# Kernel optimization log

Hardware: AMD Instinct MI355X
Metric: run time of the kernel (lower is better)

## Reference

```python
import jax, jax.numpy as jnp
import numpy as np

START_INDEX = 1


def _lstm_cell(x, h, c, W_ih, W_hh, b_ih, b_hh):
    # PyTorch LSTM cell: gate order i, f, g, o
    gates = x @ W_ih.T + b_ih + h @ W_hh.T + b_hh  # [B, 4H]
    i, f, g, o = jnp.split(gates, 4, axis=-1)
    c_new = jax.nn.sigmoid(f) * c + jax.nn.sigmoid(i) * jnp.tanh(g)
    h_new = jax.nn.sigmoid(o) * jnp.tanh(c_new)
    return h_new, c_new


def setup_inputs() -> dict:
    key = jax.random.key(0)
    ks = jax.random.split(key, 13)
    B, C, E, H, V = 32, 512, 512, 512, 32000
    s = 0.05  # keep gates in non-saturated range

    def w(k, shape):
        return jax.random.normal(k, shape, dtype=jnp.float32) * s

    return {
        "context": jax.random.normal(ks[0], (B, C), dtype=jnp.float32),
        "emb": w(ks[1], (V, E)),
        "W_ih_l0": w(ks[2], (4 * H, E + C)),
        "W_hh_l0": w(ks[3], (4 * H, H)),
        "b_ih_l0": w(ks[4], (4 * H,)),
        "b_hh_l0": w(ks[5], (4 * H,)),
        "W_ih_l1": w(ks[6], (4 * H, H)),
        "W_hh_l1": w(ks[7], (4 * H, H)),
        "b_ih_l1": w(ks[8], (4 * H,)),
        "b_hh_l1": w(ks[9], (4 * H,)),
        "W_out": w(ks[10], (V, H)),
        "b_out": w(ks[11], (V,)),
        "max_len": 64,
    }


def reference(context, emb, W_ih_l0, W_hh_l0, b_ih_l0, b_hh_l0,
              W_ih_l1, W_hh_l1, b_ih_l1, b_hh_l1, W_out, b_out, max_len):
    B = context.shape[0]
    H = W_hh_l0.shape[1]
    tok0 = jnp.full((B,), START_INDEX, dtype=jnp.int32)
    z = jnp.zeros((B, H), dtype=context.dtype)

    def step(carry, _):
        tok, h0, c0, h1, c1 = carry
        ex = emb[tok]                                   # [B, E] embedding lookup
        inp = jnp.concatenate([ex, context], axis=-1)   # [B, E+C]
        h0, c0 = _lstm_cell(inp, h0, c0, W_ih_l0, W_hh_l0, b_ih_l0, b_hh_l0)
        h1, c1 = _lstm_cell(h0, h1, c1, W_ih_l1, W_hh_l1, b_ih_l1, b_hh_l1)
        logits = h1 @ W_out.T + b_out                   # [B, V]
        logp = jax.nn.log_softmax(logits, axis=-1)
        tok_next = jnp.argmax(logp, axis=-1).astype(jnp.int32)  # greedy feedback (detached)
        return (tok_next, h0, c0, h1, c1), logp

    _, out = jax.lax.scan(step, (tok0, z, z, z, z), None, length=max_len)
    return jnp.transpose(out, (1, 0, 2))                # [B, max_len, V]
```

## Files before the change

kernel.cpp:

```cpp
#include <hip/hip_runtime.h>
#include <math.h>

#define BB 32
#define HH 512
#define VV 32000
#define TT 64
#define NTILE 1000

#define OFF_H0T   0
#define OFF_H1T   32768
#define OFF_C0    65536
#define OFF_C1    81920
#define OFF_PC0   98304
#define OFF_AMAX  163840
#define OFF_PAIRS 163904

typedef float f32x4_ __attribute__((ext_vector_type(4)));

__device__ __forceinline__ float sigmoidf_(float x) { return 1.0f / (1.0f + expf(-x)); }

__device__ __forceinline__ float dot4(const float4 wv, const float4 xv) {
    return wv.x * xv.x + wv.y * xv.y + wv.z * xv.z + wv.w * xv.w;
}
__device__ __forceinline__ void bcast_fma(float* A, const float4 wv,
                                          const float4 x0, const float4 x1,
                                          const float4 x2, const float4 x3) {
    A[0] += wv.x * x0.x + wv.y * x1.x + wv.z * x2.x + wv.w * x3.x;
    A[1] += wv.x * x0.y + wv.y * x1.y + wv.z * x2.y + wv.w * x3.y;
    A[2] += wv.x * x0.z + wv.y * x1.z + wv.z * x2.z + wv.w * x3.z;
    A[3] += wv.x * x0.w + wv.y * x1.w + wv.z * x2.w + wv.w * x3.w;
}

__global__ void k_init(float* __restrict__ ws) {
    int idx = blockIdx.x * 256 + threadIdx.x;
    ws[OFF_H0T + idx] = 0.0f;
    ws[OFF_H1T + idx] = 0.0f;
    ws[OFF_C0 + idx]  = 0.0f;
    ws[OFF_C1 + idx]  = 0.0f;
    if (idx < BB) ((unsigned long long*)(ws + OFF_AMAX))[idx] = 0xFFFFFFFEull;
}

__global__ __launch_bounds__(256, 4) void k_pc0(
    const float* __restrict__ Wih0, const float* __restrict__ ctx,
    const float* __restrict__ bih0, const float* __restrict__ bhh0,
    float* __restrict__ pc0)
{
    __shared__ float red[16][16][32];
    const int tid = threadIdx.x;
    const int ks = tid >> 4, bg = (tid >> 2) & 3, rg = tid & 3;
    const int hu = blockIdx.x * 4 + rg;
    const int k0 = ks * 32, b0 = bg * 8;

    float acc[4][8];
#pragma unroll
    for (int g = 0; g < 4; ++g)
#pragma unroll
        for (int j = 0; j < 8; ++j) acc[g][j] = 0.0f;

    const float* wp[4];
#pragma unroll
    for (int g = 0; g < 4; ++g) wp[g] = Wih0 + (size_t)(g * 512 + hu) * 1024 + 512 + k0;

#pragma unroll 2
    for (int kk4 = 0; kk4 < 8; ++kk4) {
        const int kk = kk4 * 4;
        float4 w4[4];
#pragma unroll
        for (int g = 0; g < 4; ++g) w4[g] = *(const float4*)(wp[g] + kk);
#pragma unroll
        for (int j = 0; j < 8; ++j) {
            const float4 xe = *(const float4*)(ctx + (size_t)(b0 + j) * 512 + k0 + kk);
#pragma unroll
            for (int g = 0; g < 4; ++g) acc[g][j] += dot4(w4[g], xe);
        }
    }

#pragma unroll
    for (int g = 0; g < 4; ++g) {
        *(float4*)&red[ks][g * 4 + rg][b0]     = make_float4(acc[g][0], acc[g][1], acc[g][2], acc[g][3]);
        *(float4*)&red[ks][g * 4 + rg][b0 + 4] = make_float4(acc[g][4], acc[g][5], acc[g][6], acc[g][7]);
    }
    __syncthreads();
    if (tid < 128) {
        const int huL = (tid >> 5) & 3, b = tid & 31;
#pragma unroll
        for (int g = 0; g < 4; ++g) {
            float s = 0.0f;
#pragma unroll
            for (int k = 0; k < 16; ++k) s += red[k][g * 4 + huL][b];
            const int row = g * 512 + blockIdx.x * 4 + huL;
            pc0[(size_t)row * 32 + b] = s + bih0[row] + bhh0[row];
        }
    }
}

template <int MODE>
__global__ __launch_bounds__(256, 4) void k_lstm(
    const float* __restrict__ Wa, const float* __restrict__ Wb,
    const float* __restrict__ xA, const float* __restrict__ xB,
    const float* __restrict__ emb,
    const unsigned long long* __restrict__ amax_in,
    const float* __restrict__ pc0,
    const float* __restrict__ bih, const float* __restrict__ bhh,
    float* __restrict__ hT_out, float* __restrict__ c_st,
    unsigned long long* __restrict__ amax_reset)
{
    constexpr int SA = (MODE == 0) ? 1024 : 512;
    __shared__ float red[16][8][32];

    const int tid = threadIdx.x;
    const int ks = tid >> 4, bg = (tid >> 1) & 7, rg = tid & 1;
    const int hu = blockIdx.x * 2 + rg;
    const int b0 = bg * 4;
    const bool partA = (ks < 8);
    const int k0 = (partA ? ks : ks - 8) * 64;

    float acc[4][4];
#pragma unroll
    for (int g = 0; g < 4; ++g)
#pragma unroll
        for (int j = 0; j < 4; ++j) acc[g][j] = 0.0f;

    const float* wp[4];
#pragma unroll
    for (int g = 0; g < 4; ++g)
        wp[g] = partA ? (Wa + (size_t)(g * 512 + hu) * SA + k0)
                      : (Wb + (size_t)(g * 512 + hu) * 512 + k0);

    const float* ep[4];
    if (MODE == 0 && partA) {
#pragma unroll
        for (int j = 0; j < 4; ++j) {
            const int tok = (int)(0xFFFFFFFFu - (unsigned)(amax_in[b0 + j] & 0xFFFFFFFFull));
            ep[j] = emb + (size_t)tok * 512 + k0;
        }
    }
    const float* xb = (partA ? xA : xB) + (size_t)k0 * 32 + b0;

#pragma unroll 2
    for (int kk4 = 0; kk4 < 16; ++kk4) {
        const int kk = kk4 * 4;
        float4 w4[4];
#pragma unroll
        for (int g = 0; g < 4; ++g) w4[g] = *(const float4*)(wp[g] + kk);
        if (MODE == 0 && partA) {
#pragma unroll
            for (int j = 0; j < 4; ++j) {
                const float4 xe = *(const float4*)(ep[j] + kk);
#pragma unroll
                for (int g = 0; g < 4; ++g) acc[g][j] += dot4(w4[g], xe);
            }
        } else {
            const float4 x0 = *(const float4*)(xb + (size_t)(kk + 0) * 32);
            const float4 x1 = *(const float4*)(xb + (size_t)(kk + 1) * 32);
            const float4 x2 = *(const float4*)(xb + (size_t)(kk + 2) * 32);
            const float4 x3 = *(const float4*)(xb + (size_t)(kk + 3) * 32);
#pragma unroll
            for (int g = 0; g < 4; ++g) bcast_fma(acc[g], w4[g], x0, x1, x2, x3);
        }
    }

#pragma unroll
    for (int g = 0; g < 4; ++g)
        *(float4*)&red[ks][g * 2 + rg][b0] = make_float4(acc[g][0], acc[g][1], acc[g][2], acc[g][3]);
    __syncthreads();

    if (tid < 64) {
        const int huL = tid >> 5, b = tid & 31;
        const int hu2 = blockIdx.x * 2 + huL;
        float gate[4];
#pragma unroll
        for (int g = 0; g < 4; ++g) {
            float s = 0.0f;
#pragma unroll
            for (int k = 0; k < 16; ++k) s += red[k][g * 2 + huL][b];
            const int row = g * 512 + hu2;
            if (MODE == 0) s += pc0[(size_t)row * 32 + b];
            else           s += bih[row] + bhh[row];
            gate[g] = s;
        }
        const float gi = sigmoidf_(gate[0]);
        const float gf = sigmoidf_(gate[1]);
        const float gg = tanhf(gate[2]);
        const float go = sigmoidf_(gate[3]);
        const int ci = hu2 * 32 + b;
        const float cn = gf * c_st[ci] + gi * gg;
        c_st[ci] = cn;
        hT_out[ci] = go * tanhf(cn);
    }
    if (MODE == 1) {
        if (tid >= 64 && tid < 96) amax_reset[tid - 64] = 0ull;
    }
}

__global__ __launch_bounds__(256, 4) void k_logits(
    const float* __restrict__ h1T, const float* __restrict__ Wout,
    const float* __restrict__ bout, float* __restrict__ out,
    unsigned long long* __restrict__ amax, float* __restrict__ pairs, int t)
{
    __shared__ float red[8][32][36];
    __shared__ unsigned long long lmax[8][32];
    __shared__ float pm[8][32], ps[8][32];

    const int tid = threadIdx.x;
    const int rg = tid & 7, bg = (tid >> 3) & 3, ks = tid >> 5;
    const int row0 = blockIdx.x * 32 + rg * 4;
    const int b0 = bg * 8, k0 = ks * 64;

    float acc[4][8];
#pragma unroll
    for (int i = 0; i < 4; ++i)
#pragma unroll
        for (int j = 0; j < 8; ++j) acc[i][j] = 0.0f;

    const float* wp[4];
#pragma unroll
    for (int i = 0; i < 4; ++i) wp[i] = Wout + (size_t)(row0 + i) * 512 + k0;
    const float* xb = h1T + (size_t)k0 * 32 + b0;

#pragma unroll 2
    for (int kk4 = 0; kk4 < 16; ++kk4) {
        const int kk = kk4 * 4;
        const float4 x00 = *(const float4*)(xb + (size_t)(kk + 0) * 32);
        const float4 x01 = *(const float4*)(xb + (size_t)(kk + 0) * 32 + 4);
        const float4 x10 = *(const float4*)(xb + (size_t)(kk + 1) * 32);
        const float4 x11 = *(const float4*)(xb + (size_t)(kk + 1) * 32 + 4);
        const float4 x20 = *(const float4*)(xb + (size_t)(kk + 2) * 32);
        const float4 x21 = *(const float4*)(xb + (size_t)(kk + 2) * 32 + 4);
        const float4 x30 = *(const float4*)(xb + (size_t)(kk + 3) * 32);
        const float4 x31 = *(const float4*)(xb + (size_t)(kk + 3) * 32 + 4);
#pragma unroll
        for (int i = 0; i < 4; ++i) {
            const float4 w = *(const float4*)(wp[i] + kk);
            bcast_fma(&acc[i][0], w, x00, x10, x20, x30);
            bcast_fma(&acc[i][4], w, x01, x11, x21, x31);
        }
    }

#pragma unroll
    for (int i = 0; i < 4; ++i) {
        *(float4*)&red[ks][rg * 4 + i][b0]     = make_float4(acc[i][0], acc[i][1], acc[i][2], acc[i][3]);
        *(float4*)&red[ks][rg * 4 + i][b0 + 4] = make_float4(acc[i][4], acc[i][5], acc[i][6], acc[i][7]);
    }
    __syncthreads();

    {
        const int r2 = tid & 31, bq = tid >> 5;
        const int row = blockIdx.x * 32 + r2;
        const float bias = bout[row];
#pragma unroll
        for (int j = 0; j < 4; ++j) {
            const int b = bq * 4 + j;
            float v = bias;
#pragma unroll
            for (int k = 0; k < 8; ++k) v += red[k][r2][b];
            out[((size_t)b * TT + t) * VV + row] = v;
        }
    }
    {
        const int b = tid & 31, rq = tid >> 5;
        unsigned long long best = 0ull;
        float vv[4];
#pragma unroll
        for (int i = 0; i < 4; ++i) {
            const int rr = rq * 4 + i;
            const int row = blockIdx.x * 32 + rr;
            float v = bout[row];
#pragma unroll
            for (int k = 0; k < 8; ++k) v += red[k][rr][b];
            vv[i] = v;
            unsigned u = __float_as_uint(v);
            u = (u & 0x80000000u) ? ~u : (u | 0x80000000u);
            const unsigned long long key =
                ((unsigned long long)u << 32) | (unsigned long long)(0xFFFFFFFFu - (unsigned)row);
            best = best > key ? best : key;
        }
        lmax[rq][b] = best;
        const float lm = fmaxf(fmaxf(vv[0], vv[1]), fmaxf(vv[2], vv[3]));
        ps[rq][b] = __expf(vv[0] - lm) + __expf(vv[1] - lm)
                  + __expf(vv[2] - lm) + __expf(vv[3] - lm);
        pm[rq][b] = lm;
    }
    __syncthreads();
    if (tid < 32) {
        unsigned long long bb = lmax[0][tid];
#pragma unroll
        for (int q = 1; q < 8; ++q) bb = bb > lmax[q][tid] ? bb : lmax[q][tid];
        if (bb > amax[tid]) atomicMax(&amax[tid], bb);
        if (pairs) {
            float M = pm[0][tid], S = ps[0][tid];
#pragma unroll
            for (int q = 1; q < 8; ++q) {
                const float nm = fmaxf(M, pm[q][tid]);
                S = S * __expf(M - nm) + ps[q][tid] * __expf(pm[q][tid] - nm);
                M = nm;
            }
            float* pr = pairs + ((size_t)t * NTILE + blockIdx.x) * 64;
            pr[tid] = M;
            pr[32 + tid] = S;
        }
    }
}

__global__ __launch_bounds__(256) void k_lsm(float* __restrict__ out,
                                             const float* __restrict__ pairs) {
    float* p = out + (size_t)blockIdx.x * VV;
    const int tid = threadIdx.x;
    __shared__ float sm[4], ss[4];

    float m = -1e30f, s = 0.0f;
    if (pairs) {
        const int b = blockIdx.x >> 6, t = blockIdx.x & 63;
        const float* pr = pairs + (size_t)t * NTILE * 64 + b;
        for (int tile = tid; tile < NTILE; tile += 256) {
            const float tm = pr[(size_t)tile * 64];
            const float ts = pr[(size_t)tile * 64 + 32];
            const float nm = fmaxf(m, tm);
            s = s * __expf(m - nm) + ts * __expf(tm - nm);
            m = nm;
        }
    } else {
        for (int i = tid * 4; i < VV; i += 1024) {
            const float4 v = *(const float4*)(p + i);
            const float cm = fmaxf(fmaxf(v.x, v.y), fmaxf(v.z, v.w));
            const float nm = fmaxf(m, cm);
            s = s * __expf(m - nm) + __expf(v.x - nm) + __expf(v.y - nm)
                                   + __expf(v.z - nm) + __expf(v.w - nm);
            m = nm;
        }
    }
#pragma unroll
    for (int off = 32; off > 0; off >>= 1) {
        const float om = __shfl_down(m, off, 64);
        const float os = __shfl_down(s, off, 64);
        const float nm = fmaxf(m, om);
        s = s * __expf(m - nm) + os * __expf(om - nm);
        m = nm;
    }
    if ((tid & 63) == 0) { sm[tid >> 6] = m; ss[tid >> 6] = s; }
    __syncthreads();
    float M = sm[0], S = ss[0];
#pragma unroll
    for (int w = 1; w < 4; ++w) {
        const float nm = fmaxf(M, sm[w]);
        S = S * __expf(M - nm) + ss[w] * __expf(sm[w] - nm);
        M = nm;
    }
    const float lz = M + __logf(S);
    for (int i = tid * 4; i < VV; i += 1024) {
        f32x4_ v = *(const f32x4_*)(p + i);
        v = v - lz;
        __builtin_nontemporal_store(v, (f32x4_*)(p + i));
    }
}

extern "C" void kernel_launch(void* const* d_in, const int* in_sizes, int n_in,
                              void* d_out, int out_size, void* d_ws, size_t ws_size,
                              hipStream_t stream) {
    const float* ctx  = (const float*)d_in[0];
    const float* emb  = (const float*)d_in[1];
    const float* Wih0 = (const float*)d_in[2];
    const float* Whh0 = (const float*)d_in[3];
    const float* bih0 = (const float*)d_in[4];
    const float* bhh0 = (const float*)d_in[5];
    const float* Wih1 = (const float*)d_in[6];
    const float* Whh1 = (const float*)d_in[7];
    const float* bih1 = (const float*)d_in[8];
    const float* bhh1 = (const float*)d_in[9];
    const float* Wout = (const float*)d_in[10];
    const float* bout = (const float*)d_in[11];

    float* out = (float*)d_out;
    float* ws  = (float*)d_ws;
    float* h0T[2] = { ws + OFF_H0T, ws + OFF_H0T + 16384 };
    float* h1T[2] = { ws + OFF_H1T, ws + OFF_H1T + 16384 };
    float* c0  = ws + OFF_C0;
    float* c1  = ws + OFF_C1;
    float* pc0 = ws + OFF_PC0;
    unsigned long long* amax = (unsigned long long*)(ws + OFF_AMAX);

    const size_t need_bytes = (size_t)(OFF_PAIRS + TT * NTILE * 64) * sizeof(float);
    float* pairs = (ws_size >= need_bytes) ? (ws + OFF_PAIRS) : nullptr;

    k_init<<<64, 256, 0, stream>>>(ws);
    k_pc0<<<128, 256, 0, stream>>>(Wih0, ctx, bih0, bhh0, pc0);

    for (int t = 0; t < TT; ++t) {
        const int pp = t & 1, nn = pp ^ 1;
        k_lstm<0><<<256, 256, 0, stream>>>(
            Wih0, Whh0, nullptr, h0T[pp], emb, amax, pc0, nullptr, nullptr,
            h0T[nn], c0, nullptr);
        k_lstm<1><<<256, 256, 0, stream>>>(
            Wih1, Whh1, h0T[nn], h1T[pp], emb, nullptr, nullptr, bih1, bhh1,
            h1T[nn], c1, amax);
        k_logits<<<1000, 256, 0, stream>>>(h1T[nn], Wout, bout, out, amax, pairs, t);
    }
    k_lsm<<<BB * TT, 256, 0, stream>>>(out, pairs);
}
```

Before: 5.452 ms.

## Fuse per-step decode kernels into one persistent kernel with grid barriers

Replaces the 192 per-timestep launches (two LSTM layers plus logits, 64 steps) with a single persistent 256-block kernel. The three phases are separated by a custom flag-based global barrier, and the argmax buffer is double-buffered so no reset kernel is needed. The LSTM and logits tiling is remapped to 512-thread blocks with wavefront shuffle reductions in place of shared-memory reductions. The logits phase uses 250 blocks of 128 rows and fuses the partial softmax statistics. The aim is to remove launch overhead and inter-kernel gaps. The costs are spin-wait barrier latency, reliance on all 256 blocks being co-resident, and fewer blocks for the large Wout GEMV.

```diff
diff --git a/kernel.cpp b/kernel.cpp
--- a/kernel.cpp
+++ b/kernel.cpp
@@ -5,15 +5,20 @@
 #define HH 512
 #define VV 32000
 #define TT 64
-#define NTILE 1000
+#define GRID 256
+#define NLOG 250
+#define RPB 128
+
+typedef unsigned long long ull;
 
 #define OFF_H0T   0
 #define OFF_H1T   32768
 #define OFF_C0    65536
 #define OFF_C1    81920
 #define OFF_PC0   98304
-#define OFF_AMAX  163840
-#define OFF_PAIRS 163904
+#define OFF_AMAX2 163840
+#define OFF_BAR   163968
+#define OFF_PAIRS 164480
 
 typedef float f32x4_ __attribute__((ext_vector_type(4)));
 
@@ -37,7 +42,10 @@
     ws[OFF_H1T + idx] = 0.0f;
     ws[OFF_C0 + idx]  = 0.0f;
     ws[OFF_C1 + idx]  = 0.0f;
-    if (idx < BB) ((unsigned long long*)(ws + OFF_AMAX))[idx] = 0xFFFFFFFEull;
+    if (idx < 64) {
+        ((ull*)(ws + OFF_AMAX2))[idx] = (idx < 32) ? 0xFFFFFFFEull : 0ull;
+    }
+    if (idx < 512) ((unsigned*)(ws + OFF_BAR))[idx] = 0u;
 }
 
 __global__ __launch_bounds__(256, 4) void k_pc0(
@@ -94,26 +102,49 @@
     }
 }
 
+__device__ __forceinline__ void gbar(unsigned* flags, unsigned* done, unsigned target) {
+    __syncthreads();
+    if (threadIdx.x == 0) {
+        __threadfence();
+        atomicExch(&flags[blockIdx.x], target);
+    }
+    if (blockIdx.x == 0 && threadIdx.x < 64) {
+#pragma unroll
+        for (int i = 0; i < GRID / 64; ++i) {
+            unsigned* f = &flags[i * 64 + threadIdx.x];
+            while (atomicAdd(f, 0u) < target) __builtin_amdgcn_s_sleep(1);
+        }
+        if (threadIdx.x < 4) atomicExch(&done[threadIdx.x * 32], target);
+    }
+    if (threadIdx.x == 0 && blockIdx.x != 0) {
+        unsigned* d = &done[(blockIdx.x & 3) * 32];
+        while (atomicAdd(d, 0u) < target) __builtin_amdgcn_s_sleep(1);
+    }
+    if (threadIdx.x == 0) __threadfence();
+    __syncthreads();
+}
+
 template <int MODE>
-__global__ __launch_bounds__(256, 4) void k_lstm(
+__device__ __forceinline__ void lstm_phase(
+    const int blk, const int tid,
     const float* __restrict__ Wa, const float* __restrict__ Wb,
     const float* __restrict__ xA, const float* __restrict__ xB,
     const float* __restrict__ emb,
-    const unsigned long long* __restrict__ amax_in,
+    const ull* __restrict__ amax_rd,
     const float* __restrict__ pc0,
     const float* __restrict__ bih, const float* __restrict__ bhh,
     float* __restrict__ hT_out, float* __restrict__ c_st,
-    unsigned long long* __restrict__ amax_reset)
+    ull* __restrict__ amax_zero,
+    float (*__restrict__ part)[4][32])
 {
     constexpr int SA = (MODE == 0) ? 1024 : 512;
-    __shared__ float red[16][8][32];
-
-    const int tid = threadIdx.x;
-    const int ks = tid >> 4, bg = (tid >> 1) & 7, rg = tid & 1;
-    const int hu = blockIdx.x * 2 + rg;
-    const int b0 = bg * 4;
-    const bool partA = (ks < 8);
-    const int k0 = (partA ? ks : ks - 8) * 64;
+    const int w = tid >> 6, lane = tid & 63, ks = lane >> 3, bq = lane & 7;
+    const int hu = blk * 2 + (w & 1);
+    const int c  = w >> 1;
+    const int k0 = c * 256 + ks * 32;
+    const bool partA = (k0 < 512);
+    const int ka = partA ? k0 : k0 - 512;
+    const int b0 = bq * 4;
 
     float acc[4][4];
 #pragma unroll
@@ -124,21 +155,21 @@
     const float* wp[4];
 #pragma unroll
     for (int g = 0; g < 4; ++g)
-        wp[g] = partA ? (Wa + (size_t)(g * 512 + hu) * SA + k0)
-                      : (Wb + (size_t)(g * 512 + hu) * 512 + k0);
+        wp[g] = partA ? (Wa + (size_t)(g * 512 + hu) * SA + ka)
+                      : (Wb + (size_t)(g * 512 + hu) * 512 + ka);
 
     const float* ep[4];
     if (MODE == 0 && partA) {
 #pragma unroll
         for (int j = 0; j < 4; ++j) {
-            const int tok = (int)(0xFFFFFFFFu - (unsigned)(amax_in[b0 + j] & 0xFFFFFFFFull));
-            ep[j] = emb + (size_t)tok * 512 + k0;
-        }
-    }
-    const float* xb = (partA ? xA : xB) + (size_t)k0 * 32 + b0;
-
-#pragma unroll 2
-    for (int kk4 = 0; kk4 < 16; ++kk4) {
+            const int tok = (int)(0xFFFFFFFFu - (unsigned)(amax_rd[b0 + j] & 0xFFFFFFFFull));
+            ep[j] = emb + (size_t)tok * 512 + ka;
+        }
+    }
+    const float* xp = (partA ? xA : xB) + (size_t)ka * 32 + b0;
+
+#pragma unroll
+    for (int kk4 = 0; kk4 < 8; ++kk4) {
         const int kk = kk4 * 4;
         float4 w4[4];
 #pragma unroll
@@ -151,154 +182,187 @@
                 for (int g = 0; g < 4; ++g) acc[g][j] += dot4(w4[g], xe);
             }
         } else {
+            const float4 x0 = *(const float4*)(xp + (size_t)(kk + 0) * 32);
+            const float4 x1 = *(const float4*)(xp + (size_t)(kk + 1) * 32);
+            const float4 x2 = *(const float4*)(xp + (size_t)(kk + 2) * 32);
+            const float4 x3 = *(const float4*)(xp + (size_t)(kk + 3) * 32);
+#pragma unroll
+            for (int g = 0; g < 4; ++g) bcast_fma(acc[g], w4[g], x0, x1, x2, x3);
+        }
+    }
+
+#pragma unroll
+    for (int off = 8; off <= 32; off <<= 1)
+#pragma unroll
+        for (int g = 0; g < 4; ++g)
+#pragma unroll
+            for (int j = 0; j < 4; ++j)
+                acc[g][j] += __shfl_xor(acc[g][j], off, 64);
+
+    if (ks < 4)
+        *(float4*)&part[w][ks][b0] = make_float4(acc[ks][0], acc[ks][1], acc[ks][2], acc[ks][3]);
+
+    if (MODE == 0 && blk == GRID - 1 && tid >= 64 && tid < 96)
+        amax_zero[tid - 64] = 0ull;
+
+    __syncthreads();
+
+    if (tid < 64) {
+        const int hl = tid >> 5, b = tid & 31;
+        const int hu2 = blk * 2 + hl;
+        float gate[4];
+#pragma unroll
+        for (int g = 0; g < 4; ++g) {
+            float s = part[hl][g][b] + part[2 + hl][g][b]
+                    + part[4 + hl][g][b] + part[6 + hl][g][b];
+            const int row = g * 512 + hu2;
+            s += (MODE == 0) ? pc0[(size_t)row * 32 + b] : (bih[row] + bhh[row]);
+            gate[g] = s;
+        }
+        const float gi = sigmoidf_(gate[0]);
+        const float gf = sigmoidf_(gate[1]);
+        const float gn = tanhf(gate[2]);
+        const float go = sigmoidf_(gate[3]);
+        const int ci = hu2 * 32 + b;
+        const float cn = gf * c_st[ci] + gi * gn;
+        c_st[ci] = cn;
+        hT_out[ci] = go * tanhf(cn);
+    }
+}
+
+__device__ __forceinline__ void logits_phase(
+    const int blk, const int tid, const int t,
+    const float* __restrict__ h1, const float* __restrict__ Wout,
+    const float* __restrict__ bout, float* __restrict__ out,
+    ull* __restrict__ amax_wr, float* __restrict__ pairs,
+    float (*__restrict__ trans)[33])
+{
+    if (blk >= NLOG) return;
+    const int w = tid >> 6, lane = tid & 63, ks = lane >> 3, bq = lane & 7;
+    const int row0 = blk * RPB;
+    const int b0 = bq * 4, k0 = ks * 64;
+    const float* xb = h1 + (size_t)k0 * 32 + b0;
+
+#pragma unroll
+    for (int pass = 0; pass < 2; ++pass) {
+        const int rbase = w * 16 + pass * 8;
+        const float* wbase = Wout + (size_t)(row0 + rbase) * 512 + k0;
+        float acc[8][4];
+#pragma unroll
+        for (int r = 0; r < 8; ++r)
+#pragma unroll
+            for (int j = 0; j < 4; ++j) acc[r][j] = 0.0f;
+
+#pragma unroll 4
+        for (int kk4 = 0; kk4 < 16; ++kk4) {
+            const int kk = kk4 * 4;
             const float4 x0 = *(const float4*)(xb + (size_t)(kk + 0) * 32);
             const float4 x1 = *(const float4*)(xb + (size_t)(kk + 1) * 32);
             const float4 x2 = *(const float4*)(xb + (size_t)(kk + 2) * 32);
             const float4 x3 = *(const float4*)(xb + (size_t)(kk + 3) * 32);
 #pragma unroll
-            for (int g = 0; g < 4; ++g) bcast_fma(acc[g], w4[g], x0, x1, x2, x3);
-        }
-    }
-
-#pragma unroll
-    for (int g = 0; g < 4; ++g)
-        *(float4*)&red[ks][g * 2 + rg][b0] = make_float4(acc[g][0], acc[g][1], acc[g][2], acc[g][3]);
-    __syncthreads();
-
-    if (tid < 64) {
-        const int huL = tid >> 5, b = tid & 31;
-        const int hu2 = blockIdx.x * 2 + huL;
-        float gate[4];
-#pragma unroll
-        for (int g = 0; g < 4; ++g) {
-            float s = 0.0f;
-#pragma unroll
-            for (int k = 0; k < 16; ++k) s += red[k][g * 2 + huL][b];
-            const int row = g * 512 + hu2;
-            if (MODE == 0) s += pc0[(size_t)row * 32 + b];
-            else           s += bih[row] + bhh[row];
-            gate[g] = s;
-        }
-        const float gi = sigmoidf_(gate[0]);
-        const float gf = sigmoidf_(gate[1]);
-        const float gg = tanhf(gate[2]);
-        const float go = sigmoidf_(gate[3]);
-        const int ci = hu2 * 32 + b;
-        const float cn = gf * c_st[ci] + gi * gg;
-        c_st[ci] = cn;
-        hT_out[ci] = go * tanhf(cn);
-    }
-    if (MODE == 1) {
-        if (tid >= 64 && tid < 96) amax_reset[tid - 64] = 0ull;
-    }
-}
-
-__global__ __launch_bounds__(256, 4) void k_logits(
-    const float* __restrict__ h1T, const float* __restrict__ Wout,
+            for (int r = 0; r < 8; ++r) {
+                const float4 w4 = *(const float4*)(wbase + (size_t)r * 512 + kk);
+                bcast_fma(acc[r], w4, x0, x1, x2, x3);
+            }
+        }
+#pragma unroll
+        for (int off = 8; off <= 32; off <<= 1)
+#pragma unroll
+            for (int r = 0; r < 8; ++r)
+#pragma unroll
+                for (int j = 0; j < 4; ++j)
+                    acc[r][j] += __shfl_xor(acc[r][j], off, 64);
+
+        const float bias = bout[row0 + rbase + ks];
+#pragma unroll
+        for (int j = 0; j < 4; ++j)
+            trans[rbase + ks][b0 + j] = acc[ks][j] + bias;
+    }
+    __syncthreads();
+
+    const int b = tid >> 4, q = tid & 15;
+    const size_t obase = ((size_t)b * TT + t) * VV + row0;
+    ull best = 0ull;
+    float m = -1e30f, ssum = 0.0f;
+#pragma unroll
+    for (int h = 0; h < 2; ++h) {
+        const int r = q * 8 + h * 4;
+        float4 v;
+        v.x = trans[r + 0][b]; v.y = trans[r + 1][b];
+        v.z = trans[r + 2][b]; v.w = trans[r + 3][b];
+        *(float4*)(out + obase + r) = v;
+        const float vv[4] = { v.x, v.y, v.z, v.w };
+#pragma unroll
+        for (int i = 0; i < 4; ++i) {
+            const float x = vv[i];
+            unsigned u = __float_as_uint(x);
+            u = (u & 0x80000000u) ? ~u : (u | 0x80000000u);
+            const unsigned row = (unsigned)(row0 + r + i);
+            const ull key = ((ull)u << 32) | (ull)(0xFFFFFFFFu - row);
+            best = best > key ? best : key;
+            const float nm = fmaxf(m, x);
+            ssum = ssum * __expf(m - nm) + __expf(x - nm);
+            m = nm;
+        }
+    }
+#pragma unroll
+    for (int off = 1; off < 16; off <<= 1) {
+        const ull ob = __shfl_xor(best, off, 64);
+        best = best > ob ? best : ob;
+        const float om = __shfl_xor(m, off, 64);
+        const float os = __shfl_xor(ssum, off, 64);
+        const float nm = fmaxf(m, om);
+        ssum = ssum * __expf(m - nm) + os * __expf(om - nm);
+        m = nm;
+    }
+    if (q == 0) {
+        atomicMax(&amax_wr[b], best);
+        if (pairs) {
+            float* pr = pairs + ((size_t)t * NLOG + blk) * 64;
+            pr[b] = m;
+            pr[32 + b] = ssum;
+        }
+    }
+}
+
+__global__ __launch_bounds__(512) void k_decode(
+    const float* __restrict__ Wih0, const float* __restrict__ Whh0,
+    const float* __restrict__ Wih1, const float* __restrict__ Whh1,
+    const float* __restrict__ bih1, const float* __restrict__ bhh1,
+    const float* __restrict__ emb,  const float* __restrict__ Wout,
     const float* __restrict__ bout, float* __restrict__ out,
-    unsigned long long* __restrict__ amax, float* __restrict__ pairs, int t)
+    float* __restrict__ ws, int use_pairs)
 {
-    __shared__ float red[8][32][36];
-    __shared__ unsigned long long lmax[8][32];
-    __shared__ float pm[8][32], ps[8][32];
-
-    const int tid = threadIdx.x;
-    const int rg = tid & 7, bg = (tid >> 3) & 3, ks = tid >> 5;
-    const int row0 = blockIdx.x * 32 + rg * 4;
-    const int b0 = bg * 8, k0 = ks * 64;
-
-    float acc[4][8];
-#pragma unroll
-    for (int i = 0; i < 4; ++i)
-#pragma unroll
-        for (int j = 0; j < 8; ++j) acc[i][j] = 0.0f;
-
-    const float* wp[4];
-#pragma unroll
-    for (int i = 0; i < 4; ++i) wp[i] = Wout + (size_t)(row0 + i) * 512 + k0;
-    const float* xb = h1T + (size_t)k0 * 32 + b0;
-
-#pragma unroll 2
-    for (int kk4 = 0; kk4 < 16; ++kk4) {
-        const int kk = kk4 * 4;
-        const float4 x00 = *(const float4*)(xb + (size_t)(kk + 0) * 32);
-        const float4 x01 = *(const float4*)(xb + (size_t)(kk + 0) * 32 + 4);
-        const float4 x10 = *(const float4*)(xb + (size_t)(kk + 1) * 32);
-        const float4 x11 = *(const float4*)(xb + (size_t)(kk + 1) * 32 + 4);
-        const float4 x20 = *(const float4*)(xb + (size_t)(kk + 2) * 32);
-        const float4 x21 = *(const float4*)(xb + (size_t)(kk + 2) * 32 + 4);
-        const float4 x30 = *(const float4*)(xb + (size_t)(kk + 3) * 32);
-        const float4 x31 = *(const float4*)(xb + (size_t)(kk + 3) * 32 + 4);
-#pragma unroll
-        for (int i = 0; i < 4; ++i) {
-            const float4 w = *(const float4*)(wp[i] + kk);
-            bcast_fma(&acc[i][0], w, x00, x10, x20, x30);
-            bcast_fma(&acc[i][4], w, x01, x11, x21, x31);
-        }
-    }
-
-#pragma unroll
-    for (int i = 0; i < 4; ++i) {
-        *(float4*)&red[ks][rg * 4 + i][b0]     = make_float4(acc[i][0], acc[i][1], acc[i][2], acc[i][3]);
-        *(float4*)&red[ks][rg * 4 + i][b0 + 4] = make_float4(acc[i][4], acc[i][5], acc[i][6], acc[i][7]);
-    }
-    __syncthreads();
-
-    {
-        const int r2 = tid & 31, bq = tid >> 5;
-        const int row = blockIdx.x * 32 + r2;
-        const float bias = bout[row];
-#pragma unroll
-        for (int j = 0; j < 4; ++j) {
-            const int b = bq * 4 + j;
-            float v = bias;
-#pragma unroll
-            for (int k = 0; k < 8; ++k) v += red[k][r2][b];
-            out[((size_t)b * TT + t) * VV + row] = v;
-        }
-    }
-    {
-        const int b = tid & 31, rq = tid >> 5;
-        unsigned long long best = 0ull;
-        float vv[4];
-#pragma unroll
-        for (int i = 0; i < 4; ++i) {
-            const int rr = rq * 4 + i;
-            const int row = blockIdx.x * 32 + rr;
-            float v = bout[row];
-#pragma unroll
-            for (int k = 0; k < 8; ++k) v += red[k][rr][b];
-            vv[i] = v;
-            unsigned u = __float_as_uint(v);
-            u = (u & 0x80000000u) ? ~u : (u | 0x80000000u);
-            const unsigned long long key =
-                ((unsigned long long)u << 32) | (unsigned long long)(0xFFFFFFFFu - (unsigned)row);
-            best = best > key ? best : key;
-        }
-        lmax[rq][b] = best;
-        const float lm = fmaxf(fmaxf(vv[0], vv[1]), fmaxf(vv[2], vv[3]));
-        ps[rq][b] = __expf(vv[0] - lm) + __expf(vv[1] - lm)
-                  + __expf(vv[2] - lm) + __expf(vv[3] - lm);
-        pm[rq][b] = lm;
-    }
-    __syncthreads();
-    if (tid < 32) {
-        unsigned long long bb = lmax[0][tid];
-#pragma unroll
-        for (int q = 1; q < 8; ++q) bb = bb > lmax[q][tid] ? bb : lmax[q][tid];
-        if (bb > amax[tid]) atomicMax(&amax[tid], bb);
-        if (pairs) {
-            float M = pm[0][tid], S = ps[0][tid];
-#pragma unroll
-            for (int q = 1; q < 8; ++q) {
-                const float nm = fmaxf(M, pm[q][tid]);
-                S = S * __expf(M - nm) + ps[q][tid] * __expf(pm[q][tid] - nm);
-                M = nm;
-            }
-            float* pr = pairs + ((size_t)t * NTILE + blockIdx.x) * 64;
-            pr[tid] = M;
-            pr[32 + tid] = S;
-        }
+    __shared__ float s_part[8][4][32];
+    __shared__ float s_trans[RPB][33];
+
+    const int blk = blockIdx.x, tid = threadIdx.x;
+    float* h0a = ws + OFF_H0T;  float* h0b = h0a + 16384;
+    float* h1a = ws + OFF_H1T;  float* h1b = h1a + 16384;
+    float* c0  = ws + OFF_C0;   float* c1  = ws + OFF_C1;
+    const float* pc0 = ws + OFF_PC0;
+    ull* amax2 = (ull*)(ws + OFF_AMAX2);
+    unsigned* flags = (unsigned*)(ws + OFF_BAR);
+    unsigned* done  = flags + 320;
+    float* pairs = use_pairs ? (ws + OFF_PAIRS) : nullptr;
+
+    unsigned bar = 0;
+    for (int t = 0; t < TT; ++t) {
+        const int pp = t & 1;
+        float* h0p = pp ? h0b : h0a;  float* h0n = pp ? h0a : h0b;
+        float* h1p = pp ? h1b : h1a;  float* h1n = pp ? h1a : h1b;
+        ull* amax_rd = amax2 + (size_t)(t & 1) * 32;
+        ull* amax_wr = amax2 + (size_t)((t + 1) & 1) * 32;
+
+        lstm_phase<0>(blk, tid, Wih0, Whh0, emb, h0p, emb,
+                      amax_rd, pc0, nullptr, nullptr, h0n, c0, amax_wr, s_part);
+        gbar(flags, done, ++bar);
+        lstm_phase<1>(blk, tid, Wih1, Whh1, h0n, h1p, nullptr,
+                      nullptr, nullptr, bih1, bhh1, h1n, c1, nullptr, s_part);
+        gbar(flags, done, ++bar);
+        logits_phase(blk, tid, t, h1n, Wout, bout, out, amax_wr, pairs, s_trans);
+        gbar(flags, done, ++bar);
     }
 }
 
@@ -311,8 +375,8 @@
     float m = -1e30f, s = 0.0f;
     if (pairs) {
         const int b = blockIdx.x >> 6, t = blockIdx.x & 63;
-        const float* pr = pairs + (size_t)t * NTILE * 64 + b;
-        for (int tile = tid; tile < NTILE; tile += 256) {
+        const float* pr = pairs + (size_t)t * NLOG * 64 + b;
+        for (int tile = tid; tile < NLOG; tile += 256) {
             const float tm = pr[(size_t)tile * 64];
             const float ts = pr[(size_t)tile * 64 + 32];
             const float nm = fmaxf(m, tm);
@@ -372,28 +436,13 @@
 
     float* out = (float*)d_out;
     float* ws  = (float*)d_ws;
-    float* h0T[2] = { ws + OFF_H0T, ws + OFF_H0T + 16384 };
-    float* h1T[2] = { ws + OFF_H1T, ws + OFF_H1T + 16384 };
-    float* c0  = ws + OFF_C0;
-    float* c1  = ws + OFF_C1;
-    float* pc0 = ws + OFF_PC0;
-    unsigned long long* amax = (unsigned long long*)(ws + OFF_AMAX);
-
-    const size_t need_bytes = (size_t)(OFF_PAIRS + TT * NTILE * 64) * sizeof(float);
-    float* pairs = (ws_size >= need_bytes) ? (ws + OFF_PAIRS) : nullptr;
+
+    const size_t need_bytes = (size_t)(OFF_PAIRS + (size_t)TT * NLOG * 64) * sizeof(float);
+    const int use_pairs = (ws_size >= need_bytes) ? 1 : 0;
 
     k_init<<<64, 256, 0, stream>>>(ws);
-    k_pc0<<<128, 256, 0, stream>>>(Wih0, ctx, bih0, bhh0, pc0);
-
-    for (int t = 0; t < TT; ++t) {
-        const int pp = t & 1, nn = pp ^ 1;
-        k_lstm<0><<<256, 256, 0, stream>>>(
-            Wih0, Whh0, nullptr, h0T[pp], emb, amax, pc0, nullptr, nullptr,
-            h0T[nn], c0, nullptr);
-        k_lstm<1><<<256, 256, 0, stream>>>(
-            Wih1, Whh1, h0T[nn], h1T[pp], emb, nullptr, nullptr, bih1, bhh1,
-            h1T[nn], c1, amax);
-        k_logits<<<1000, 256, 0, stream>>>(h1T[nn], Wout, bout, out, amax, pairs, t);
-    }
-    k_lsm<<<BB * TT, 256, 0, stream>>>(out, pairs);
-}
+    k_pc0<<<128, 256, 0, stream>>>(Wih0, ctx, bih0, bhh0, ws + OFF_PC0);
+    k_decode<<<GRID, 512, 0, stream>>>(Wih0, Whh0, Wih1, Whh1, bih1, bhh1,
+                                       emb, Wout, bout, out, ws, use_pairs);
+    k_lsm<<<BB * TT, 256, 0, stream>>>(out, use_pairs ? (ws + OFF_PAIRS) : nullptr);
+}
```

New measurement: 11.81 ms. 117% more time.
